# Performance work log

Measured on AMD Instinct MI355X. Metric: run time of the kernel, lower is better.

## Reference

```python
import jax, jax.numpy as jnp
import numpy as np

N_NODES = 100000
N_EDGES = 1600000
IN_FEATS = 128
HID = 32
N_REL = 5
N_BASES = 2
N_PAIRS = 4096


def setup_inputs() -> dict:
    key = jax.random.key(0)
    ks = jax.random.split(key, 24)
    d = {}
    d['x'] = jax.random.normal(ks[0], (N_NODES, IN_FEATS), dtype=jnp.float32)
    d['edge_mask'] = jnp.ones((N_EDGES,), dtype=jnp.float32)
    d['etype'] = jax.random.randint(ks[1], (N_EDGES,), 0, N_REL, dtype=jnp.int32)
    d['src'] = jax.random.randint(ks[2], (N_EDGES,), 0, N_NODES, dtype=jnp.int32)
    d['dst'] = jax.random.randint(ks[3], (N_EDGES,), 0, N_NODES, dtype=jnp.int32)
    d['users_idx'] = jax.random.randint(ks[4], (N_PAIRS,), 0, N_NODES, dtype=jnp.int32)
    d['items_idx'] = jax.random.randint(ks[5], (N_PAIRS,), 0, N_NODES, dtype=jnp.int32)
    # RelGraphConv params (basis decomposition): layer1 in->32, layers 2,3 32->32
    def s(k, din):
        return 1.0 / np.sqrt(din)
    d['V1'] = jax.random.normal(ks[6], (N_BASES, IN_FEATS, HID), dtype=jnp.float32) * s(0, IN_FEATS)
    d['comp1'] = jax.random.normal(ks[7], (N_REL, N_BASES), dtype=jnp.float32)
    d['loop1'] = jax.random.normal(ks[8], (IN_FEATS, HID), dtype=jnp.float32) * s(0, IN_FEATS)
    d['b1'] = jnp.zeros((HID,), dtype=jnp.float32)
    d['V2'] = jax.random.normal(ks[9], (N_BASES, HID, HID), dtype=jnp.float32) * s(0, HID)
    d['comp2'] = jax.random.normal(ks[10], (N_REL, N_BASES), dtype=jnp.float32)
    d['loop2'] = jax.random.normal(ks[11], (HID, HID), dtype=jnp.float32) * s(0, HID)
    d['b2'] = jnp.zeros((HID,), dtype=jnp.float32)
    d['V3'] = jax.random.normal(ks[12], (N_BASES, HID, HID), dtype=jnp.float32) * s(0, HID)
    d['comp3'] = jax.random.normal(ks[13], (N_REL, N_BASES), dtype=jnp.float32)
    d['loop3'] = jax.random.normal(ks[14], (HID, HID), dtype=jnp.float32) * s(0, HID)
    d['b3'] = jnp.zeros((HID,), dtype=jnp.float32)
    # MLP head: lin1 (2*sum(latent_dim[1:]) = 192 -> 128), lin2 (128 -> 1)
    d['w1'] = jax.random.normal(ks[15], (2 * 3 * HID, 128), dtype=jnp.float32) * (1.0 / np.sqrt(2 * 3 * HID))
    d['bw1'] = jnp.zeros((128,), dtype=jnp.float32)
    d['w2'] = jax.random.normal(ks[16], (128, 1), dtype=jnp.float32) * (1.0 / np.sqrt(128))
    d['bw2'] = jnp.zeros((1,), dtype=jnp.float32)
    return d


def _rgcn_layer(x, V, comp, loopw, bias, etype, src, dst, norm):
    # basis-decomposed relational conv: W_r = sum_b comp[r,b] * V[b]
    xb = jnp.einsum('nd,bdo->nbo', x, V)                       # [N,B,O]
    msg = jnp.einsum('eb,ebo->eo', comp[etype], xb[src])       # [E,O]
    msg = msg * norm[:, None]                                  # edge_mask norm
    agg = jax.ops.segment_sum(msg, dst, num_segments=x.shape[0])
    return jnp.tanh(agg + x @ loopw + bias)


def reference(x, edge_mask, etype, src, dst, users_idx, items_idx,
              V1, comp1, loop1, b1, V2, comp2, loop2, b2, V3, comp3, loop3, b3,
              w1, bw1, w2, bw2):
    h1 = _rgcn_layer(x, V1, comp1, loop1, b1, etype, src, dst, edge_mask)
    h2 = _rgcn_layer(h1, V2, comp2, loop2, b2, etype, src, dst, edge_mask)
    h3 = _rgcn_layer(h2, V3, comp3, loop3, b3, etype, src, dst, edge_mask)
    concat_states = jnp.concatenate([h1, h2, h3], axis=1)      # [N, 96]
    feats = jnp.concatenate([concat_states[users_idx], concat_states[items_idx]], axis=1)  # [P,192]
    hidden = jax.nn.relu(feats @ w1 + bw1)
    out = hidden @ w2 + bw2
    return out[:, 0]  # multiply_by = 1
```

## Files before the change

kernel.cpp:

```cpp
#include <hip/hip_runtime.h>
#include <stdint.h>

#define N_NODES  100000
#define N_EDGES  1600000
#define IN_FEATS 128
#define HID      32
#define N_REL    5
#define N_BASES  2
#define N_PAIRS  4096

#define NB        196
#define BSCAT_BLOCKS 391
#define NGROUPS   6250

typedef __attribute__((ext_vector_type(8))) short short8;
typedef __attribute__((ext_vector_type(4))) float f32x4;

__device__ inline unsigned int pack_bf16(float a, float b) {
    unsigned int ua = __float_as_uint(a), ub = __float_as_uint(b);
    ua = (ua + 0x7fffu + ((ua >> 16) & 1u)) >> 16;
    ub = (ub + 0x7fffu + ((ub >> 16) & 1u)) >> 16;
    return ua | (ub << 16);
}

__device__ inline unsigned short bf16_1(float a) {
    unsigned int u = __float_as_uint(a);
    u = (u + 0x7fffu + ((u >> 16) & 1u)) >> 16;
    return (unsigned short)u;
}


__global__ __launch_bounds__(256) void k_pre(
    const float* __restrict__ V1, const float* __restrict__ comp1, const float* __restrict__ loop1,
    const float* __restrict__ V2, const float* __restrict__ comp2, const float* __restrict__ loop2,
    const float* __restrict__ V3, const float* __restrict__ comp3, const float* __restrict__ loop3,
    unsigned short* __restrict__ Wbf1, unsigned short* __restrict__ Wbf2,
    unsigned short* __restrict__ Wbf3,
    const int* __restrict__ dst, int* __restrict__ ghist) {
    __shared__ int lh[NB];
    int b = blockIdx.x;
    int t = threadIdx.x;
    if (b < 144) {
        const float *V, *comp, *loopw;
        unsigned short* Wbf;
        int D, idx;
        if (b < 96)      { V = V1; comp = comp1; loopw = loop1; Wbf = Wbf1; D = IN_FEATS; idx = b * 256 + t; }
        else if (b < 120){ V = V2; comp = comp2; loopw = loop2; Wbf = Wbf2; D = HID;      idx = (b - 96) * 256 + t; }
        else             { V = V3; comp = comp3; loopw = loop3; Wbf = Wbf3; D = HID;      idx = (b - 120) * 256 + t; }
        if (idx >= 192 * D) return;
        int j = idx / D, k = idx % D;
        float v;
        if (j < 160) {
            int r = j >> 5, o = j & 31;
            v = comp[r * 2 + 0] * V[(size_t)(0 * D + k) * 32 + o]
              + comp[r * 2 + 1] * V[(size_t)(1 * D + k) * 32 + o];
        } else {
            v = loopw[k * 32 + (j - 160)];
        }
        Wbf[idx] = bf16_1(v);
    } else {
        int blk = b - 144;
        for (int i = t; i < NB; i += 256) lh[i] = 0;
        __syncthreads();
        int e0 = blk * 4096;
#pragma unroll
        for (int i = 0; i < 16; i++) {
            int e = e0 + t + i * 256;
            if (e < N_EDGES) atomicAdd(&lh[dst[e] >> 9], 1);
        }
        __syncthreads();
        for (int i = t; i < NB; i += 256) {
            int c = lh[i];
            if (c) atomicAdd(&ghist[i], c);
        }
    }
}


__global__ __launch_bounds__(256) void k_bscatter(
    const int* __restrict__ src, const int* __restrict__ dst,
    const int* __restrict__ etype, const float* __restrict__ mask,
    const int* __restrict__ ghist, int* __restrict__ gcur, int2* __restrict__ ebuf) {
    __shared__ int lh[NB];
    __shared__ int lbase[NB];
    __shared__ int bs[NB];
    int t = threadIdx.x;
    if (t < NB) lh[t] = 0;
    __syncthreads();
    int e0 = blockIdx.x * 4096;
#pragma unroll
    for (int i = 0; i < 16; i++) {
        int e = e0 + t + i * 256;
        if (e < N_EDGES) atomicAdd(&lh[dst[e] >> 9], 1);
    }
    __syncthreads();
    int gv = 0, c = 0;
    if (t < NB) { gv = ghist[t]; c = lh[t]; bs[t] = gv; }
    __syncthreads();
    for (int off = 1; off < 256; off <<= 1) {
        int v = 0;
        if (t < NB && t >= off) v = bs[t - off];
        __syncthreads();
        if (t < NB) bs[t] += v;
        __syncthreads();
    }
    if (t < NB) {
        int excl = bs[t] - gv;
        lbase[t] = excl + (c ? atomicAdd(&gcur[t], c) : 0);
        lh[t] = 0;
    }
    __syncthreads();
#pragma unroll
    for (int i = 0; i < 16; i++) {
        int e = e0 + t + i * 256;
        if (e < N_EDGES) {
            int d = dst[e];
            int b = d >> 9;
            int r = atomicAdd(&lh[b], 1);
            int2 pk;
            pk.x = ((d & 511) << 23) | (src[e] * 80 + etype[e] * 16);
            pk.y = __float_as_int(mask[e]);
            ebuf[lbase[b] + r] = pk;
        }
    }
}


__global__ __launch_bounds__(1024) void k_bsort(
    const int* __restrict__ ghist, const int2* __restrict__ ebuf,
    int2* __restrict__ esort, int* __restrict__ offsets) {
    __shared__ int hist[512];
    __shared__ int incl[512];
    __shared__ int cur[512];
    __shared__ int bs[256];
    __shared__ int sS0, sS1;
    int b = blockIdx.x, t = threadIdx.x;
    if (t < 256) bs[t] = (t < NB) ? ghist[t] : 0;
    __syncthreads();
    for (int off = 1; off < 256; off <<= 1) {
        int v = 0;
        if (t < 256 && t >= off) v = bs[t - off];
        __syncthreads();
        if (t < 256) bs[t] += v;
        __syncthreads();
    }
    if (t == 0) { sS1 = bs[b]; sS0 = bs[b] - ghist[b]; }
    if (t < 512) hist[t] = 0;
    __syncthreads();
    int s0 = sS0, s1 = sS1;
    for (int e = s0 + t; e < s1; e += 1024) {
        int dl = ((unsigned)ebuf[e].x) >> 23;
        atomicAdd(&hist[dl], 1);
    }
    __syncthreads();
    if (t < 512) incl[t] = hist[t];
    __syncthreads();
    for (int off = 1; off < 512; off <<= 1) {
        int v = 0;
        if (t < 512 && t >= off) v = incl[t - off];
        __syncthreads();
        if (t < 512) incl[t] += v;
        __syncthreads();
    }
    if (t < 512) {
        int ex = incl[t] - hist[t];
        cur[t] = ex;
        int n = (b << 9) + t;
        if (n <= N_NODES) offsets[n] = s0 + ex;
    }
    if (b == NB - 1 && t == 0) offsets[N_NODES] = N_EDGES;
    __syncthreads();
    for (int e = s0 + t; e < s1; e += 1024) {
        int2 pk = ebuf[e];
        int dl = ((unsigned)pk.x) >> 23;
        int pos = s0 + atomicAdd(&cur[dl], 1);
        int2 rec;
        rec.x = pk.x & 0x7fffff;
        rec.y = pk.y;
        esort[pos] = rec;
    }
}


__global__ __launch_bounds__(256) void k_transform_l1(
    const float* __restrict__ xin,
    const unsigned short* __restrict__ Wbf, const float* __restrict__ bias,
    unsigned int* __restrict__ xrel16, float* __restrict__ aggout) {
    __shared__ unsigned short As[16 * 136];
    int t = threadIdx.x;
    int wv = t >> 6, lane = t & 63;
    int q = lane >> 4, n16 = lane & 15;
    short8 bfr[3][4];
#pragma unroll
    for (int i = 0; i < 3; i++) {
        int tt = wv * 3 + i;
#pragma unroll
        for (int ks = 0; ks < 4; ks++)
            bfr[i][ks] = *(const short8*)(Wbf + (tt * 16 + n16) * 128 + ks * 32 + q * 8);
    }
    float bv0 = bias[n16], bv1 = bias[16 + n16];
    int node_l = t >> 4;
    int seg    = t & 15;
    unsigned short* xs16 = (unsigned short*)xrel16;
    int g0 = blockIdx.x * 5;
    float4 p0, p1;
    {
        const float* xr = xin + ((size_t)(g0 * 16 + node_l)) * 128 + seg * 8;
        p0 = *(const float4*)xr;
        p1 = *(const float4*)(xr + 4);
    }
    for (int gi = 0; gi < 5; gi++) {
        int g = g0 + gi;
        int n0 = g * 16;
        __syncthreads();
        {
            unsigned int u0 = pack_bf16(p0.x, p0.y);
            unsigned int u1 = pack_bf16(p0.z, p0.w);
            unsigned int u2 = pack_bf16(p1.x, p1.y);
            unsigned int u3 = pack_bf16(p1.z, p1.w);
            uint4 v; v.x = u0; v.y = u1; v.z = u2; v.w = u3;
            *(uint4*)(As + node_l * 136 + seg * 8) = v;
        }
        __syncthreads();
        if (gi + 1 < 5) {
            const float* xr = xin + ((size_t)((g + 1) * 16 + node_l)) * 128 + seg * 8;
            p0 = *(const float4*)xr;
            p1 = *(const float4*)(xr + 4);
        }
        short8 afr[4];
#pragma unroll
        for (int ks = 0; ks < 4; ks++)
            afr[ks] = *(const short8*)(As + n16 * 136 + ks * 32 + q * 8);
        f32x4 d[3];
        f32x4 z = {0.f, 0.f, 0.f, 0.f};
#pragma unroll
        for (int i = 0; i < 3; i++) d[i] = z;
#pragma unroll
        for (int i = 0; i < 3; i++)
#pragma unroll
            for (int ks = 0; ks < 4; ks++)
                d[i] = __builtin_amdgcn_mfma_f32_16x16x32_bf16(afr[ks], bfr[i][ks], d[i], 0, 0, 0);
#pragma unroll
        for (int i = 0; i < 3; i++) {
            int tt = wv * 3 + i;
            if (tt < 10) {
#pragma unroll
                for (int r = 0; r < 4; r++) {
                    int node = n0 + q * 4 + r;
                    xs16[(size_t)node * 160 + tt * 16 + n16] = bf16_1(d[i][r]);
                }
            } else {
                float bv = (tt == 10) ? bv0 : bv1;
                int o = (tt - 10) * 16 + n16;
#pragma unroll
                for (int r = 0; r < 4; r++) {
                    int node = n0 + q * 4 + r;
                    aggout[(size_t)node * 32 + o] = d[i][r] + bv;
                }
            }
        }
    }
}


__global__ __launch_bounds__(256) void k_transform_reg32(
    const float* __restrict__ xin, int xstride,
    const unsigned short* __restrict__ Wbf, const float* __restrict__ bias,
    unsigned int* __restrict__ xrel16, float* __restrict__ aggout) {
    int t = threadIdx.x;
    int wv = t >> 6, lane = t & 63;
    int q = lane >> 4, n16 = lane & 15;
    short8 bfr[12];
#pragma unroll
    for (int t12 = 0; t12 < 12; t12++)
        bfr[t12] = *(const short8*)(Wbf + (t12 * 16 + n16) * 32 + q * 8);
    float bv0 = bias[n16], bv1 = bias[16 + n16];
    unsigned short* xs16 = (unsigned short*)xrel16;
    int gstep = gridDim.x * 4;
    int g = blockIdx.x * 4 + wv;
    float4 x0, x1;
    if (g < NGROUPS) {
        const float* xr = xin + (size_t)(g * 16 + n16) * xstride + q * 8;
        x0 = *(const float4*)(xr);
        x1 = *(const float4*)(xr + 4);
    }
    while (g < NGROUPS) {
        int gn = g + gstep;
        union { unsigned int u[4]; short8 s; } cv;
        cv.u[0] = pack_bf16(x0.x, x0.y);
        cv.u[1] = pack_bf16(x0.z, x0.w);
        cv.u[2] = pack_bf16(x1.x, x1.y);
        cv.u[3] = pack_bf16(x1.z, x1.w);
        short8 afr = cv.s;
        float4 nx0, nx1;
        if (gn < NGROUPS) {
            const float* xr = xin + (size_t)(gn * 16 + n16) * xstride + q * 8;
            nx0 = *(const float4*)(xr);
            nx1 = *(const float4*)(xr + 4);
        }
        f32x4 d[12];
        f32x4 z = {0.f, 0.f, 0.f, 0.f};
#pragma unroll
        for (int i = 0; i < 12; i++) d[i] = z;
#pragma unroll
        for (int t12 = 0; t12 < 12; t12++)
            d[t12] = __builtin_amdgcn_mfma_f32_16x16x32_bf16(afr, bfr[t12], d[t12], 0, 0, 0);
        int n0 = g * 16;
#pragma unroll
        for (int t12 = 0; t12 < 10; t12++) {
#pragma unroll
            for (int r = 0; r < 4; r++) {
                int node = n0 + q * 4 + r;
                xs16[(size_t)node * 160 + t12 * 16 + n16] = bf16_1(d[t12][r]);
            }
        }
#pragma unroll
        for (int r = 0; r < 4; r++) {
            int node = n0 + q * 4 + r;
            aggout[(size_t)node * 32 + n16]      = d[10][r] + bv0;
            aggout[(size_t)node * 32 + 16 + n16] = d[11][r] + bv1;
        }
        x0 = nx0; x1 = nx1; g = gn;
    }
}


__global__ __launch_bounds__(256) void k_agg(
    const int* __restrict__ offsets, const int2* __restrict__ esort,
    const unsigned int* __restrict__ xrel16, const float* __restrict__ agg,
    float* __restrict__ hout, int hoff) {
    int v = blockIdx.x * 32 + (threadIdx.x >> 3);
    int o = threadIdx.x & 7;
    if (v >= N_NODES) return;
    int s0 = offsets[v], s1 = offsets[v + 1];
    float4 a0 = *(const float4*)(agg + (size_t)v * 32 + o * 4);
    float acc0 = a0.x, acc1 = a0.y, acc2 = a0.z, acc3 = a0.w;
    int last = s1 - 1;
    for (int e = s0; e < s1; e += 8) {
        int addr[8];
        float m[8];
#pragma unroll
        for (int i = 0; i < 8; i++) {
            int ei = e + i;
            int ec = (ei <= last) ? ei : last;
            int2 pk = esort[ec];
            addr[i] = pk.x;
            m[i] = (ei <= last) ? __int_as_float(pk.y) : 0.f;
        }
        uint2 xw[8];
#pragma unroll
        for (int i = 0; i < 8; i++)
            xw[i] = *(const uint2*)(xrel16 + (unsigned)addr[i] + o * 2);
#pragma unroll
        for (int i = 0; i < 8; i++) {
            float f0 = __uint_as_float(xw[i].x << 16);
            float f1 = __uint_as_float(xw[i].x & 0xffff0000u);
            float f2 = __uint_as_float(xw[i].y << 16);
            float f3 = __uint_as_float(xw[i].y & 0xffff0000u);
            acc0 = fmaf(m[i], f0, acc0);
            acc1 = fmaf(m[i], f1, acc1);
            acc2 = fmaf(m[i], f2, acc2);
            acc3 = fmaf(m[i], f3, acc3);
        }
    }
    float4 r;
    r.x = tanhf(acc0); r.y = tanhf(acc1); r.z = tanhf(acc2); r.w = tanhf(acc3);
    *(float4*)(hout + (size_t)v * 96 + hoff + o * 4) = r;
}


__global__ void k_mlp(const float* __restrict__ concat, const int* __restrict__ uidx,
                      const int* __restrict__ iidx,
                      const float* __restrict__ w1, const float* __restrict__ bw1,
                      const float* __restrict__ w2, const float* __restrict__ bw2,
                      float* __restrict__ out) {
    __shared__ float feats[192];
    __shared__ float red[2];
    int p = blockIdx.x;
    int t = threadIdx.x;
    int u = uidx[p], it = iidx[p];
    for (int k = t; k < 192; k += 128)
        feats[k] = (k < 96) ? concat[(size_t)u * 96 + k] : concat[(size_t)it * 96 + (k - 96)];
    __syncthreads();
    float acc = bw1[t];
    for (int k = 0; k < 192; k++) acc += feats[k] * w1[k * 128 + t];
    float h = fmaxf(acc, 0.f);
    float part = h * w2[t];
    for (int off = 32; off > 0; off >>= 1) part += __shfl_down(part, off, 64);
    if ((t & 63) == 0) red[t >> 6] = part;
    __syncthreads();
    if (t == 0) out[p] = red[0] + red[1] + bw2[0];
}


extern "C" void kernel_launch(void* const* d_in, const int* in_sizes, int n_in,
                              void* d_out, int out_size, void* d_ws, size_t ws_size,
                              hipStream_t stream) {
    const float* x         = (const float*)d_in[0];
    const float* edge_mask = (const float*)d_in[1];
    const int*   etype     = (const int*)d_in[2];
    const int*   src       = (const int*)d_in[3];
    const int*   dst       = (const int*)d_in[4];
    const int*   users_idx = (const int*)d_in[5];
    const int*   items_idx = (const int*)d_in[6];
    const float* V1        = (const float*)d_in[7];
    const float* comp1     = (const float*)d_in[8];
    const float* loop1     = (const float*)d_in[9];
    const float* b1        = (const float*)d_in[10];
    const float* V2        = (const float*)d_in[11];
    const float* comp2     = (const float*)d_in[12];
    const float* loop2     = (const float*)d_in[13];
    const float* b2        = (const float*)d_in[14];
    const float* V3        = (const float*)d_in[15];
    const float* comp3     = (const float*)d_in[16];
    const float* loop3     = (const float*)d_in[17];
    const float* b3        = (const float*)d_in[18];
    const float* w1        = (const float*)d_in[19];
    const float* bw1       = (const float*)d_in[20];
    const float* w2        = (const float*)d_in[21];
    const float* bw2       = (const float*)d_in[22];
    float* out = (float*)d_out;

    uintptr_t w = (uintptr_t)d_ws;
    auto al = [&](size_t bytes) { uintptr_t p = (w + 255) & ~(uintptr_t)255; w = p + bytes; return p; };
    int*   ghist   = (int*)al(sizeof(int) * 2 * NB);
    int*   gcur    = ghist + NB;
    int*   offsets = (int*)al(sizeof(int) * (N_NODES + 1));
    uintptr_t big0 = al(sizeof(unsigned int) * (size_t)N_NODES * 80);
    int2*  ebuf    = (int2*)big0;
    unsigned int* xrel16 = (unsigned int*)big0;
    int2*  esort   = (int2*)al(sizeof(int2) * N_EDGES);
    unsigned short* Wbf1 = (unsigned short*)al(sizeof(unsigned short) * 192 * IN_FEATS);
    unsigned short* Wbf2 = (unsigned short*)al(sizeof(unsigned short) * 192 * HID);
    unsigned short* Wbf3 = (unsigned short*)al(sizeof(unsigned short) * 192 * HID);
    float* agg     = (float*)al(sizeof(float) * (size_t)N_NODES * 32);
    float* concat  = (float*)al(sizeof(float) * (size_t)N_NODES * 96);

    hipMemsetAsync(ghist, 0, sizeof(int) * 2 * NB, stream);

    k_pre<<<144 + BSCAT_BLOCKS, 256, 0, stream>>>(V1, comp1, loop1, V2, comp2, loop2,
                                                  V3, comp3, loop3, Wbf1, Wbf2, Wbf3,
                                                  dst, ghist);
    k_bscatter<<<BSCAT_BLOCKS, 256, 0, stream>>>(src, dst, etype, edge_mask, ghist, gcur, ebuf);
    k_bsort<<<NB, 1024, 0, stream>>>(ghist, ebuf, esort, offsets);

    const int agrid = (N_NODES + 31) / 32;

    k_transform_l1<<<1250, 256, 0, stream>>>(x, Wbf1, b1, xrel16, agg);
    k_agg<<<agrid, 256, 0, stream>>>(offsets, esort, xrel16, agg, concat, 0);

    k_transform_reg32<<<784, 256, 0, stream>>>(concat + 0, 96, Wbf2, b2, xrel16, agg);
    k_agg<<<agrid, 256, 0, stream>>>(offsets, esort, xrel16, agg, concat, 32);

    k_transform_reg32<<<784, 256, 0, stream>>>(concat + 32, 96, Wbf3, b3, xrel16, agg);
    k_agg<<<agrid, 256, 0, stream>>>(offsets, esort, xrel16, agg, concat, 64);

    k_mlp<<<N_PAIRS, 128, 0, stream>>>(concat, users_idx, items_idx, w1, bw1, w2, bw2, out);
}
```

Baseline: 368.7 us.

## Fuse edge bucket scatter with layer-1 transform and split bucket sort blocks

Merges the edge bucket-scatter and the layer-1 MFMA transform into one launch so the two independent phases run side by side. This requires giving ebuf and xrel16 separate workspace buffers, where they previously aliased. The scatter now uses smaller 2048-edge blocks, and the per-bucket sort is split across two 512-thread blocks, each handling half the local destinations. The aggregation gather unroll goes from 8 to 16 edges to keep more loads in flight. The costs are extra workspace memory, redundant histogramming in the two sort halves, and higher register pressure in k_agg.

```diff
diff --git a/kernel.cpp b/kernel.cpp
--- a/kernel.cpp
+++ b/kernel.cpp
@@ -10,7 +10,8 @@
 #define N_PAIRS  4096
 
 #define NB        196
-#define BSCAT_BLOCKS 391
+#define BS2       782
+#define T1BLKS    1250
 #define NGROUPS   6250
 
 typedef __attribute__((ext_vector_type(8))) short short8;
@@ -77,56 +78,135 @@
 }
 
 
-__global__ __launch_bounds__(256) void k_bscatter(
+__global__ __launch_bounds__(256) void k_fuseB(
     const int* __restrict__ src, const int* __restrict__ dst,
     const int* __restrict__ etype, const float* __restrict__ mask,
-    const int* __restrict__ ghist, int* __restrict__ gcur, int2* __restrict__ ebuf) {
-    __shared__ int lh[NB];
-    __shared__ int lbase[NB];
-    __shared__ int bs[NB];
+    const int* __restrict__ ghist, int* __restrict__ gcur, int2* __restrict__ ebuf,
+    const float* __restrict__ xin, const unsigned short* __restrict__ Wbf,
+    const float* __restrict__ bias,
+    unsigned short* __restrict__ xs16, float* __restrict__ aggout) {
     int t = threadIdx.x;
-    if (t < NB) lh[t] = 0;
-    __syncthreads();
-    int e0 = blockIdx.x * 4096;
-#pragma unroll
-    for (int i = 0; i < 16; i++) {
-        int e = e0 + t + i * 256;
-        if (e < N_EDGES) atomicAdd(&lh[dst[e] >> 9], 1);
-    }
-    __syncthreads();
-    int gv = 0, c = 0;
-    if (t < NB) { gv = ghist[t]; c = lh[t]; bs[t] = gv; }
-    __syncthreads();
-    for (int off = 1; off < 256; off <<= 1) {
-        int v = 0;
-        if (t < NB && t >= off) v = bs[t - off];
-        __syncthreads();
-        if (t < NB) bs[t] += v;
-        __syncthreads();
-    }
-    if (t < NB) {
-        int excl = bs[t] - gv;
-        lbase[t] = excl + (c ? atomicAdd(&gcur[t], c) : 0);
-        lh[t] = 0;
-    }
-    __syncthreads();
-#pragma unroll
-    for (int i = 0; i < 16; i++) {
-        int e = e0 + t + i * 256;
-        if (e < N_EDGES) {
-            int d = dst[e];
-            int b = d >> 9;
-            int r = atomicAdd(&lh[b], 1);
-            int2 pk;
-            pk.x = ((d & 511) << 23) | (src[e] * 80 + etype[e] * 16);
-            pk.y = __float_as_int(mask[e]);
-            ebuf[lbase[b] + r] = pk;
-        }
-    }
-}
-
-
-__global__ __launch_bounds__(1024) void k_bsort(
+    if (blockIdx.x < BS2) {
+        __shared__ int lh[NB];
+        __shared__ int lbase[NB];
+        __shared__ int bs[NB];
+        if (t < NB) lh[t] = 0;
+        __syncthreads();
+        int e0 = blockIdx.x * 2048;
+#pragma unroll
+        for (int i = 0; i < 8; i++) {
+            int e = e0 + t + i * 256;
+            if (e < N_EDGES) atomicAdd(&lh[dst[e] >> 9], 1);
+        }
+        __syncthreads();
+        int gv = 0, c = 0;
+        if (t < NB) { gv = ghist[t]; c = lh[t]; bs[t] = gv; }
+        __syncthreads();
+        for (int off = 1; off < 256; off <<= 1) {
+            int v = 0;
+            if (t < NB && t >= off) v = bs[t - off];
+            __syncthreads();
+            if (t < NB) bs[t] += v;
+            __syncthreads();
+        }
+        if (t < NB) {
+            int excl = bs[t] - gv;
+            lbase[t] = excl + (c ? atomicAdd(&gcur[t], c) : 0);
+            lh[t] = 0;
+        }
+        __syncthreads();
+#pragma unroll
+        for (int i = 0; i < 8; i++) {
+            int e = e0 + t + i * 256;
+            if (e < N_EDGES) {
+                int d = dst[e];
+                int b = d >> 9;
+                int r = atomicAdd(&lh[b], 1);
+                int2 pk;
+                pk.x = ((d & 511) << 23) | (src[e] * 80 + etype[e] * 16);
+                pk.y = __float_as_int(mask[e]);
+                ebuf[lbase[b] + r] = pk;
+            }
+        }
+    } else {
+        __shared__ unsigned short As[16 * 136];
+        int bi = blockIdx.x - BS2;
+        int wv = t >> 6, lane = t & 63;
+        int q = lane >> 4, n16 = lane & 15;
+        short8 bfr[3][4];
+#pragma unroll
+        for (int i = 0; i < 3; i++) {
+            int tt = wv * 3 + i;
+#pragma unroll
+            for (int ks = 0; ks < 4; ks++)
+                bfr[i][ks] = *(const short8*)(Wbf + (tt * 16 + n16) * 128 + ks * 32 + q * 8);
+        }
+        float bv0 = bias[n16], bv1 = bias[16 + n16];
+        int node_l = t >> 4;
+        int seg    = t & 15;
+        int g0 = bi * 5;
+        float4 p0, p1;
+        {
+            const float* xr = xin + ((size_t)(g0 * 16 + node_l)) * 128 + seg * 8;
+            p0 = *(const float4*)xr;
+            p1 = *(const float4*)(xr + 4);
+        }
+        for (int gi = 0; gi < 5; gi++) {
+            int g = g0 + gi;
+            int n0 = g * 16;
+            __syncthreads();
+            {
+                unsigned int u0 = pack_bf16(p0.x, p0.y);
+                unsigned int u1 = pack_bf16(p0.z, p0.w);
+                unsigned int u2 = pack_bf16(p1.x, p1.y);
+                unsigned int u3 = pack_bf16(p1.z, p1.w);
+                uint4 v; v.x = u0; v.y = u1; v.z = u2; v.w = u3;
+                *(uint4*)(As + node_l * 136 + seg * 8) = v;
+            }
+            __syncthreads();
+            if (gi + 1 < 5) {
+                const float* xr = xin + ((size_t)((g + 1) * 16 + node_l)) * 128 + seg * 8;
+                p0 = *(const float4*)xr;
+                p1 = *(const float4*)(xr + 4);
+            }
+            short8 afr[4];
+#pragma unroll
+            for (int ks = 0; ks < 4; ks++)
+                afr[ks] = *(const short8*)(As + n16 * 136 + ks * 32 + q * 8);
+            f32x4 d[3];
+            f32x4 z = {0.f, 0.f, 0.f, 0.f};
+#pragma unroll
+            for (int i = 0; i < 3; i++) d[i] = z;
+#pragma unroll
+            for (int i = 0; i < 3; i++)
+#pragma unroll
+                for (int ks = 0; ks < 4; ks++)
+                    d[i] = __builtin_amdgcn_mfma_f32_16x16x32_bf16(afr[ks], bfr[i][ks], d[i], 0, 0, 0);
+#pragma unroll
+            for (int i = 0; i < 3; i++) {
+                int tt = wv * 3 + i;
+                if (tt < 10) {
+#pragma unroll
+                    for (int r = 0; r < 4; r++) {
+                        int node = n0 + q * 4 + r;
+                        xs16[(size_t)node * 160 + tt * 16 + n16] = bf16_1(d[i][r]);
+                    }
+                } else {
+                    float bv = (tt == 10) ? bv0 : bv1;
+                    int o = (tt - 10) * 16 + n16;
+#pragma unroll
+                    for (int r = 0; r < 4; r++) {
+                        int node = n0 + q * 4 + r;
+                        aggout[(size_t)node * 32 + o] = d[i][r] + bv;
+                    }
+                }
+            }
+        }
+    }
+}
+
+
+__global__ __launch_bounds__(512) void k_bsort2(
     const int* __restrict__ ghist, const int2* __restrict__ ebuf,
     int2* __restrict__ esort, int* __restrict__ offsets) {
     __shared__ int hist[512];
@@ -134,7 +214,7 @@
     __shared__ int cur[512];
     __shared__ int bs[256];
     __shared__ int sS0, sS1;
-    int b = blockIdx.x, t = threadIdx.x;
+    int blk = blockIdx.x, b = blk >> 1, h = blk & 1, t = threadIdx.x;
     if (t < 256) bs[t] = (t < NB) ? ghist[t] : 0;
     __syncthreads();
     for (int off = 1; off < 256; off <<= 1) {
@@ -145,119 +225,40 @@
         __syncthreads();
     }
     if (t == 0) { sS1 = bs[b]; sS0 = bs[b] - ghist[b]; }
-    if (t < 512) hist[t] = 0;
+    hist[t] = 0;
     __syncthreads();
     int s0 = sS0, s1 = sS1;
-    for (int e = s0 + t; e < s1; e += 1024) {
+    for (int e = s0 + t; e < s1; e += 512) {
         int dl = ((unsigned)ebuf[e].x) >> 23;
         atomicAdd(&hist[dl], 1);
     }
     __syncthreads();
-    if (t < 512) incl[t] = hist[t];
+    incl[t] = hist[t];
     __syncthreads();
     for (int off = 1; off < 512; off <<= 1) {
         int v = 0;
-        if (t < 512 && t >= off) v = incl[t - off];
-        __syncthreads();
-        if (t < 512) incl[t] += v;
-        __syncthreads();
-    }
-    if (t < 512) {
-        int ex = incl[t] - hist[t];
-        cur[t] = ex;
+        if (t >= off) v = incl[t - off];
+        __syncthreads();
+        incl[t] += v;
+        __syncthreads();
+    }
+    int ex = incl[t] - hist[t];
+    cur[t] = ex;
+    if ((t >> 8) == h) {
         int n = (b << 9) + t;
         if (n <= N_NODES) offsets[n] = s0 + ex;
     }
-    if (b == NB - 1 && t == 0) offsets[N_NODES] = N_EDGES;
-    __syncthreads();
-    for (int e = s0 + t; e < s1; e += 1024) {
+    if (b == NB - 1 && h == 1 && t == 0) offsets[N_NODES] = N_EDGES;
+    __syncthreads();
+    for (int e = s0 + t; e < s1; e += 512) {
         int2 pk = ebuf[e];
         int dl = ((unsigned)pk.x) >> 23;
-        int pos = s0 + atomicAdd(&cur[dl], 1);
-        int2 rec;
-        rec.x = pk.x & 0x7fffff;
-        rec.y = pk.y;
-        esort[pos] = rec;
-    }
-}
-
-
-__global__ __launch_bounds__(256) void k_transform_l1(
-    const float* __restrict__ xin,
-    const unsigned short* __restrict__ Wbf, const float* __restrict__ bias,
-    unsigned int* __restrict__ xrel16, float* __restrict__ aggout) {
-    __shared__ unsigned short As[16 * 136];
-    int t = threadIdx.x;
-    int wv = t >> 6, lane = t & 63;
-    int q = lane >> 4, n16 = lane & 15;
-    short8 bfr[3][4];
-#pragma unroll
-    for (int i = 0; i < 3; i++) {
-        int tt = wv * 3 + i;
-#pragma unroll
-        for (int ks = 0; ks < 4; ks++)
-            bfr[i][ks] = *(const short8*)(Wbf + (tt * 16 + n16) * 128 + ks * 32 + q * 8);
-    }
-    float bv0 = bias[n16], bv1 = bias[16 + n16];
-    int node_l = t >> 4;
-    int seg    = t & 15;
-    unsigned short* xs16 = (unsigned short*)xrel16;
-    int g0 = blockIdx.x * 5;
-    float4 p0, p1;
-    {
-        const float* xr = xin + ((size_t)(g0 * 16 + node_l)) * 128 + seg * 8;
-        p0 = *(const float4*)xr;
-        p1 = *(const float4*)(xr + 4);
-    }
-    for (int gi = 0; gi < 5; gi++) {
-        int g = g0 + gi;
-        int n0 = g * 16;
-        __syncthreads();
-        {
-            unsigned int u0 = pack_bf16(p0.x, p0.y);
-            unsigned int u1 = pack_bf16(p0.z, p0.w);
-            unsigned int u2 = pack_bf16(p1.x, p1.y);
-            unsigned int u3 = pack_bf16(p1.z, p1.w);
-            uint4 v; v.x = u0; v.y = u1; v.z = u2; v.w = u3;
-            *(uint4*)(As + node_l * 136 + seg * 8) = v;
-        }
-        __syncthreads();
-        if (gi + 1 < 5) {
-            const float* xr = xin + ((size_t)((g + 1) * 16 + node_l)) * 128 + seg * 8;
-            p0 = *(const float4*)xr;
-            p1 = *(const float4*)(xr + 4);
-        }
-        short8 afr[4];
-#pragma unroll
-        for (int ks = 0; ks < 4; ks++)
-            afr[ks] = *(const short8*)(As + n16 * 136 + ks * 32 + q * 8);
-        f32x4 d[3];
-        f32x4 z = {0.f, 0.f, 0.f, 0.f};
-#pragma unroll
-        for (int i = 0; i < 3; i++) d[i] = z;
-#pragma unroll
-        for (int i = 0; i < 3; i++)
-#pragma unroll
-            for (int ks = 0; ks < 4; ks++)
-                d[i] = __builtin_amdgcn_mfma_f32_16x16x32_bf16(afr[ks], bfr[i][ks], d[i], 0, 0, 0);
-#pragma unroll
-        for (int i = 0; i < 3; i++) {
-            int tt = wv * 3 + i;
-            if (tt < 10) {
-#pragma unroll
-                for (int r = 0; r < 4; r++) {
-                    int node = n0 + q * 4 + r;
-                    xs16[(size_t)node * 160 + tt * 16 + n16] = bf16_1(d[i][r]);
-                }
-            } else {
-                float bv = (tt == 10) ? bv0 : bv1;
-                int o = (tt - 10) * 16 + n16;
-#pragma unroll
-                for (int r = 0; r < 4; r++) {
-                    int node = n0 + q * 4 + r;
-                    aggout[(size_t)node * 32 + o] = d[i][r] + bv;
-                }
-            }
+        if ((dl >> 8) == h) {
+            int pos = s0 + atomicAdd(&cur[dl], 1);
+            int2 rec;
+            rec.x = pk.x & 0x7fffff;
+            rec.y = pk.y;
+            esort[pos] = rec;
         }
     }
 }
@@ -266,7 +267,7 @@
 __global__ __launch_bounds__(256) void k_transform_reg32(
     const float* __restrict__ xin, int xstride,
     const unsigned short* __restrict__ Wbf, const float* __restrict__ bias,
-    unsigned int* __restrict__ xrel16, float* __restrict__ aggout) {
+    unsigned short* __restrict__ xs16, float* __restrict__ aggout) {
     int t = threadIdx.x;
     int wv = t >> 6, lane = t & 63;
     int q = lane >> 4, n16 = lane & 15;
@@ -275,7 +276,6 @@
     for (int t12 = 0; t12 < 12; t12++)
         bfr[t12] = *(const short8*)(Wbf + (t12 * 16 + n16) * 32 + q * 8);
     float bv0 = bias[n16], bv1 = bias[16 + n16];
-    unsigned short* xs16 = (unsigned short*)xrel16;
     int gstep = gridDim.x * 4;
     int g = blockIdx.x * 4 + wv;
     float4 x0, x1;
@@ -336,23 +336,23 @@
     float4 a0 = *(const float4*)(agg + (size_t)v * 32 + o * 4);
     float acc0 = a0.x, acc1 = a0.y, acc2 = a0.z, acc3 = a0.w;
     int last = s1 - 1;
-    for (int e = s0; e < s1; e += 8) {
-        int addr[8];
-        float m[8];
-#pragma unroll
-        for (int i = 0; i < 8; i++) {
+    for (int e = s0; e < s1; e += 16) {
+        int addr[16];
+        float m[16];
+#pragma unroll
+        for (int i = 0; i < 16; i++) {
             int ei = e + i;
             int ec = (ei <= last) ? ei : last;
             int2 pk = esort[ec];
             addr[i] = pk.x;
             m[i] = (ei <= last) ? __int_as_float(pk.y) : 0.f;
         }
-        uint2 xw[8];
-#pragma unroll
-        for (int i = 0; i < 8; i++)
+        uint2 xw[16];
+#pragma unroll
+        for (int i = 0; i < 16; i++)
             xw[i] = *(const uint2*)(xrel16 + (unsigned)addr[i] + o * 2);
 #pragma unroll
-        for (int i = 0; i < 8; i++) {
+        for (int i = 0; i < 16; i++) {
             float f0 = __uint_as_float(xw[i].x << 16);
             float f1 = __uint_as_float(xw[i].x & 0xffff0000u);
             float f2 = __uint_as_float(xw[i].y << 16);
@@ -426,9 +426,8 @@
     int*   ghist   = (int*)al(sizeof(int) * 2 * NB);
     int*   gcur    = ghist + NB;
     int*   offsets = (int*)al(sizeof(int) * (N_NODES + 1));
-    uintptr_t big0 = al(sizeof(unsigned int) * (size_t)N_NODES * 80);
-    int2*  ebuf    = (int2*)big0;
-    unsigned int* xrel16 = (unsigned int*)big0;
+    int2*  ebuf    = (int2*)al(sizeof(int2) * N_EDGES);
+    unsigned int* xrel16 = (unsigned int*)al(sizeof(unsigned int) * (size_t)N_NODES * 80);
     int2*  esort   = (int2*)al(sizeof(int2) * N_EDGES);
     unsigned short* Wbf1 = (unsigned short*)al(sizeof(unsigned short) * 192 * IN_FEATS);
     unsigned short* Wbf2 = (unsigned short*)al(sizeof(unsigned short) * 192 * HID);
@@ -438,21 +437,21 @@
 
     hipMemsetAsync(ghist, 0, sizeof(int) * 2 * NB, stream);
 
-    k_pre<<<144 + BSCAT_BLOCKS, 256, 0, stream>>>(V1, comp1, loop1, V2, comp2, loop2,
-                                                  V3, comp3, loop3, Wbf1, Wbf2, Wbf3,
-                                                  dst, ghist);
-    k_bscatter<<<BSCAT_BLOCKS, 256, 0, stream>>>(src, dst, etype, edge_mask, ghist, gcur, ebuf);
-    k_bsort<<<NB, 1024, 0, stream>>>(ghist, ebuf, esort, offsets);
+    k_pre<<<144 + 391, 256, 0, stream>>>(V1, comp1, loop1, V2, comp2, loop2,
+                                         V3, comp3, loop3, Wbf1, Wbf2, Wbf3,
+                                         dst, ghist);
+    k_fuseB<<<BS2 + T1BLKS, 256, 0, stream>>>(src, dst, etype, edge_mask, ghist, gcur, ebuf,
+                                              x, Wbf1, b1, (unsigned short*)xrel16, agg);
+    k_bsort2<<<2 * NB, 512, 0, stream>>>(ghist, ebuf, esort, offsets);
 
     const int agrid = (N_NODES + 31) / 32;
 
-    k_transform_l1<<<1250, 256, 0, stream>>>(x, Wbf1, b1, xrel16, agg);
     k_agg<<<agrid, 256, 0, stream>>>(offsets, esort, xrel16, agg, concat, 0);
 
-    k_transform_reg32<<<784, 256, 0, stream>>>(concat + 0, 96, Wbf2, b2, xrel16, agg);
+    k_transform_reg32<<<784, 256, 0, stream>>>(concat + 0, 96, Wbf2, b2, (unsigned short*)xrel16, agg);
     k_agg<<<agrid, 256, 0, stream>>>(offsets, esort, xrel16, agg, concat, 32);
 
-    k_transform_reg32<<<784, 256, 0, stream>>>(concat + 32, 96, Wbf3, b3, xrel16, agg);
+    k_transform_reg32<<<784, 256, 0, stream>>>(concat + 32, 96, Wbf3, b3, (unsigned short*)xrel16, agg);
     k_agg<<<agrid, 256, 0, stream>>>(offsets, esort, xrel16, agg, concat, 64);
 
     k_mlp<<<N_PAIRS, 128, 0, stream>>>(concat, users_idx, items_idx, w1, bw1, w2, bw2, out);
```

After: 390.5 us. 1.06x slower.
